# Optimization experiments

Hardware: AMD Instinct MI355X
Metric: run time of the kernel (lower is better)

The kernel has to match this reference:

```python
import jax, jax.numpy as jnp
import numpy as np

N = 100000
E = 1600000
IN_C, HID_C, OUT_C = 128, 128, 64
BN_EPS = 1e-5


def setup_inputs() -> dict:
    key = jax.random.key(0)
    ks = jax.random.split(key, 8)
    x = jax.random.normal(ks[0], (N, IN_C), dtype=jnp.float32)
    edge_index = jax.random.randint(ks[1], (2, E), 0, N, dtype=jnp.int64)
    # GCNConv: Linear(in, out, bias=False) + separate bias added after aggregation
    W1 = jax.random.normal(ks[2], (IN_C, HID_C), dtype=jnp.float32) / np.sqrt(IN_C)
    b1 = jnp.zeros((HID_C,), dtype=jnp.float32)
    gamma = jnp.ones((HID_C,), dtype=jnp.float32)
    beta = jnp.zeros((HID_C,), dtype=jnp.float32)
    W2 = jax.random.normal(ks[3], (HID_C, OUT_C), dtype=jnp.float32) / np.sqrt(HID_C)
    b2 = jnp.zeros((OUT_C,), dtype=jnp.float32)
    return {"x": x, "edge_index": edge_index, "W1": W1, "b1": b1,
            "gamma": gamma, "beta": beta, "W2": W2, "b2": b2}


def _gcn_norm(edge_index, n):
    # add self-loops, symmetric normalization deg^-1/2 * deg^-1/2 (PyG gcn_norm)
    loop = jnp.arange(n, dtype=edge_index.dtype)
    row = jnp.concatenate([edge_index[0], loop])  # source (j)
    col = jnp.concatenate([edge_index[1], loop])  # target (i)
    deg = jax.ops.segment_sum(jnp.ones_like(col, dtype=jnp.float32), col, num_segments=n)
    d_inv_sqrt = jnp.where(deg > 0, jax.lax.rsqrt(deg), 0.0)
    norm = d_inv_sqrt[row] * d_inv_sqrt[col]  # [E + N]
    return row, col, norm


def _gcn_conv(h, W, b, row, col, norm, n):
    h = h @ W                                        # [N, out]
    msg = h[row] * norm[:, None]                     # gather + scale  [E+N, out]
    agg = jax.ops.segment_sum(msg, col, num_segments=n)  # scatter-add [N, out]
    return agg + b


def _batchnorm(h, gamma, beta):
    mean = jnp.mean(h, axis=0)
    var = jnp.mean(jnp.square(h - mean), axis=0)
    return (h - mean) * jax.lax.rsqrt(var + BN_EPS) * gamma + beta


def reference(x, edge_index, W1, b1, gamma, beta, W2, b2):
    n = x.shape[0]
    row, col, norm = _gcn_norm(edge_index, n)
    h = _gcn_conv(x, W1, b1, row, col, norm, n)
    h = _batchnorm(h, gamma, beta)
    h = jax.nn.relu(h)
    # dropout is identity in deterministic/eval reference
    out = _gcn_conv(h, W2, b2, row, col, norm, n)
    return out
```

## Files before the change

kernel.cpp:

```cpp
#include <hip/hip_runtime.h>

#define IN_C 128
#define HID_C 128
#define OUT_C 64
#define BN_EPS 1e-5f
#define BUCK_SHIFT 6
#define MAXBUCK 2048

typedef unsigned short ushort_t;
typedef __attribute__((ext_vector_type(8))) short bf16x8;
typedef __attribute__((ext_vector_type(4))) float f32x4;
typedef __attribute__((ext_vector_type(8))) unsigned short u16x8;

__device__ __forceinline__ float bf2f(ushort_t u) {
  union { unsigned i; float f; } c; c.i = (unsigned)u << 16; return c.f;
}
__device__ __forceinline__ ushort_t f2bf(float f) {
  union { float f; unsigned u; } c; c.f = f;
  unsigned r = c.u + 0x7FFF + ((c.u >> 16) & 1);
  return (ushort_t)(r >> 16);
}


__global__ __launch_bounds__(256) void k_hist(const int* __restrict__ col,
                                              int* __restrict__ ghist,
                                              int e, int nbuck, int chunk) {
  __shared__ int h[MAXBUCK];
  for (int p = threadIdx.x; p < nbuck; p += 256) h[p] = 0;
  __syncthreads();
  int s = blockIdx.x * chunk;
  int t = min(s + chunk, e);
  for (int i = s + threadIdx.x; i < t; i += 256)
    atomicAdd(&h[col[i] >> BUCK_SHIFT], 1);
  __syncthreads();
  int* gh = ghist + (size_t)blockIdx.x * nbuck;
  for (int p = threadIdx.x; p < nbuck; p += 256) gh[p] = h[p];
}

__global__ __launch_bounds__(256) void k_s1(int* __restrict__ ghist,
                                            int* __restrict__ btotal, int nbuck) {
  __shared__ int sd[256];
  int p = blockIdx.x;
  int tid = threadIdx.x;
  int idx = tid * nbuck + p;
  int v = ghist[idx];
  sd[tid] = v;
  __syncthreads();
  for (int off = 1; off < 256; off <<= 1) {
    int t = (tid >= off) ? sd[tid - off] : 0;
    __syncthreads();
    sd[tid] += t;
    __syncthreads();
  }
  ghist[idx] = sd[tid] - v;
  if (tid == 255) btotal[p] = sd[255];
}

__global__ __launch_bounds__(512) void k_s2(const int* __restrict__ btotal,
                                            int* __restrict__ bstart,
                                            int nbuck, int e,
                                            int* __restrict__ rowptr, int n) {
  __shared__ int sd[512];
  int tid = threadIdx.x;
  int base = tid * 4;
  int v[4]; int s = 0;
#pragma unroll
  for (int q = 0; q < 4; q++) {
    int i = base + q;
    v[q] = (i < nbuck) ? btotal[i] : 0;
    s += v[q];
  }
  sd[tid] = s;
  __syncthreads();
  for (int off = 1; off < 512; off <<= 1) {
    int t = (tid >= off) ? sd[tid - off] : 0;
    __syncthreads();
    sd[tid] += t;
    __syncthreads();
  }
  int run = sd[tid] - s;
#pragma unroll
  for (int q = 0; q < 4; q++) {
    int i = base + q;
    if (i < nbuck) bstart[i] = run;
    run += v[q];
  }
  if (tid == 0) { bstart[nbuck] = e; rowptr[n] = e; }
}

__global__ __launch_bounds__(256) void k_scatter(const int* __restrict__ row,
                                                 const int* __restrict__ col,
                                                 const int* __restrict__ ghist,
                                                 const int* __restrict__ bstart,
                                                 unsigned* __restrict__ bpack,
                                                 int e, int nbuck, int chunk) {
  __shared__ int cur[MAXBUCK];
  const int* gh = ghist + (size_t)blockIdx.x * nbuck;
  for (int p = threadIdx.x; p < nbuck; p += 256) cur[p] = bstart[p] + gh[p];
  __syncthreads();
  int s = blockIdx.x * chunk;
  int t = min(s + chunk, e);
  for (int i = s + threadIdx.x; i < t; i += 256) {
    int c = col[i];
    int pos = atomicAdd(&cur[c >> BUCK_SHIFT], 1);
    bpack[pos] = ((unsigned)(c & 63) << 17) | (unsigned)row[i];
  }
}

__global__ __launch_bounds__(256) void k_bsort(const unsigned* __restrict__ bpack,
                                               const int* __restrict__ bstart,
                                               int* __restrict__ rowptr,
                                               float* __restrict__ dis,
                                               int* __restrict__ srcidx, int n) {
  __shared__ int cnt[64];
  __shared__ int pos[64];
  __shared__ int sbs, sbe;
  int tid = threadIdx.x;
  int p = blockIdx.x;
  if (tid < 64) cnt[tid] = 0;
  if (tid == 0) { sbs = bstart[p]; sbe = bstart[p + 1]; }
  __syncthreads();
  int bs = sbs, be = sbe;
  for (int i = bs + tid; i < be; i += 256)
    atomicAdd(&cnt[bpack[i] >> 17], 1);
  __syncthreads();
  if (tid < 64) {
    int v = cnt[tid];
    int run = v;
#pragma unroll
    for (int off = 1; off < 64; off <<= 1) {
      int o = __shfl_up(run, off, 64);
      if (tid >= off) run += o;
    }
    int excl = run - v;
    pos[tid] = excl;
    int node = (p << BUCK_SHIFT) + tid;
    if (node < n) {
      rowptr[node] = bs + excl;
      dis[node] = rsqrtf((float)(v + 1));
    }
  }
  __syncthreads();
  for (int i = bs + tid; i < be; i += 256) {
    unsigned v = bpack[i];
    int q = atomicAdd(&pos[v >> 17], 1);
    srcidx[bs + q] = (int)(v & 0x1FFFFu);
  }
}


__global__ void k_wpack(const float* __restrict__ W1, const float* __restrict__ W2,
                        ushort_t* __restrict__ WB1, ushort_t* __restrict__ WB2,
                        float* __restrict__ stats) {
  int idx = blockIdx.x * 256 + threadIdx.x;
  if (blockIdx.x == 0) stats[threadIdx.x] = 0.f;
  if (idx < 128 * 128) {
    int nn = idx >> 7, k = idx & 127;
    WB1[idx] = f2bf(W1[k * HID_C + nn]);
  }
  int idx2 = idx - 128 * 128;
  if (idx2 >= 0 && idx2 < 64 * 128) {
    int nn = idx2 >> 7, k = idx2 & 127;
    WB2[idx2] = f2bf(W2[k * OUT_C + nn]);
  }
}


__global__ __launch_bounds__(256) void k_gemm1_mfma(const float* __restrict__ x,
                                                    const ushort_t* __restrict__ WB,
                                                    ushort_t* __restrict__ h1, int n) {
  int wave = threadIdx.x >> 6;
  int lane = threadIdx.x & 63;
  int m = lane & 15;
  int kg = lane >> 4;
  int rowbase = blockIdx.x * 64 + wave * 16;
  int rrow = rowbase + m; if (rrow >= n) rrow = n - 1;
  const float* xrow = x + (size_t)rrow * IN_C + kg * 8;
  f32x4 acc[8] = {};
#pragma unroll
  for (int ks = 0; ks < 4; ks++) {
    float4 a0 = *reinterpret_cast<const float4*>(xrow + ks * 32);
    float4 a1 = *reinterpret_cast<const float4*>(xrow + ks * 32 + 4);
    bf16x8 a;
    a[0] = (short)f2bf(a0.x); a[1] = (short)f2bf(a0.y);
    a[2] = (short)f2bf(a0.z); a[3] = (short)f2bf(a0.w);
    a[4] = (short)f2bf(a1.x); a[5] = (short)f2bf(a1.y);
    a[6] = (short)f2bf(a1.z); a[7] = (short)f2bf(a1.w);
#pragma unroll
    for (int nt = 0; nt < 8; nt++) {
      bf16x8 b = *reinterpret_cast<const bf16x8*>(WB + (nt * 16 + m) * 128 + ks * 32 + kg * 8);
      acc[nt] = __builtin_amdgcn_mfma_f32_16x16x32_bf16(a, b, acc[nt], 0, 0, 0);
    }
  }
#pragma unroll
  for (int nt = 0; nt < 8; nt++)
#pragma unroll
    for (int r = 0; r < 4; r++) {
      int rowi = rowbase + kg * 4 + r;
      if (rowi < n) h1[(size_t)rowi * HID_C + nt * 16 + m] = f2bf(acc[nt][r]);
    }
}


__global__ __launch_bounds__(256) void k_gemm2_mfma(const ushort_t* __restrict__ aggb,
                                                    const ushort_t* __restrict__ WB,
                                                    const float* __restrict__ stats,
                                                    const float* __restrict__ gamma,
                                                    const float* __restrict__ beta,
                                                    ushort_t* __restrict__ h2, int n) {
  __shared__ float bnp_s[256];
  int tid = threadIdx.x;
  if (tid < 128) {
    float inv_n = 1.f / (float)n;
    float mean = stats[tid] * inv_n;
    float var = stats[128 + tid] * inv_n - mean * mean;
    float istd = rsqrtf(var + BN_EPS);
    float sc = gamma[tid] * istd;
    bnp_s[tid] = sc;
    bnp_s[128 + tid] = beta[tid] - mean * sc;
  }
  __syncthreads();
  int wave = tid >> 6;
  int lane = tid & 63;
  int m = lane & 15;
  int kg = lane >> 4;
  int rowbase = blockIdx.x * 64 + wave * 16;
  int rrow = rowbase + m; if (rrow >= n) rrow = n - 1;
  const ushort_t* arow = aggb + (size_t)rrow * HID_C + kg * 8;
  f32x4 acc[4] = {};
#pragma unroll
  for (int ks = 0; ks < 4; ks++) {
    int kbase = ks * 32 + kg * 8;
    u16x8 av = *reinterpret_cast<const u16x8*>(arow + ks * 32);
    float v[8];
#pragma unroll
    for (int q = 0; q < 8; q++)
      v[q] = bf2f(av[q]) * bnp_s[kbase + q] + bnp_s[128 + kbase + q];
    bf16x8 a;
#pragma unroll
    for (int q = 0; q < 8; q++) a[q] = (short)f2bf(v[q] > 0.f ? v[q] : 0.f);
#pragma unroll
    for (int nt = 0; nt < 4; nt++) {
      bf16x8 b = *reinterpret_cast<const bf16x8*>(WB + (nt * 16 + m) * 128 + ks * 32 + kg * 8);
      acc[nt] = __builtin_amdgcn_mfma_f32_16x16x32_bf16(a, b, acc[nt], 0, 0, 0);
    }
  }
#pragma unroll
  for (int nt = 0; nt < 4; nt++)
#pragma unroll
    for (int r = 0; r < 4; r++) {
      int rowi = rowbase + kg * 4 + r;
      if (rowi < n) h2[(size_t)rowi * OUT_C + nt * 16 + m] = f2bf(acc[nt][r]);
    }
}


__global__ __launch_bounds__(256) void k_spmm1_bf(const ushort_t* __restrict__ h,
                                                  const float* __restrict__ dis,
                                                  const int* __restrict__ rowptr,
                                                  const int* __restrict__ srcidx,
                                                  const float* __restrict__ bias,
                                                  ushort_t* __restrict__ outp, int n) {
  constexpr int C = HID_C;
  constexpr int LPR = C / 8;
  constexpr int ROWS = 256 / LPR;
  int tid = threadIdx.x;
  int lane = tid & (LPR - 1);
  int r = tid / LPR;
  int i = blockIdx.x * ROWS + r;
  if (i >= n) return;
  int c8 = lane * 8;
  const ushort_t* hb = h + c8;

  float di = dis[i];
  float acc[8];
  u16x8 hv = *reinterpret_cast<const u16x8*>(hb + (size_t)i * C);
#pragma unroll
  for (int q = 0; q < 8; q++) acc[q] = di * bf2f(hv[q]);

  int s = rowptr[i], t = rowptr[i + 1];
  int p = s;
  for (; p + 16 <= t; p += 16) {
    int jA[8], jB[8]; float dA[8], dB[8]; u16x8 vA[8], vB[8];
#pragma unroll
    for (int k = 0; k < 8; k++) jA[k] = srcidx[p + k];
#pragma unroll
    for (int k = 0; k < 8; k++) jB[k] = srcidx[p + 8 + k];
#pragma unroll
    for (int k = 0; k < 8; k++) dA[k] = dis[jA[k]];
#pragma unroll
    for (int k = 0; k < 8; k++) dB[k] = dis[jB[k]];
#pragma unroll
    for (int k = 0; k < 8; k++)
      vA[k] = *reinterpret_cast<const u16x8*>(hb + (size_t)jA[k] * C);
#pragma unroll
    for (int k = 0; k < 8; k++)
      vB[k] = *reinterpret_cast<const u16x8*>(hb + (size_t)jB[k] * C);
#pragma unroll
    for (int k = 0; k < 8; k++)
#pragma unroll
      for (int q = 0; q < 8; q++) acc[q] += dA[k] * bf2f(vA[k][q]);
#pragma unroll
    for (int k = 0; k < 8; k++)
#pragma unroll
      for (int q = 0; q < 8; q++) acc[q] += dB[k] * bf2f(vB[k][q]);
  }
  for (; p + 4 <= t; p += 4) {
    int j[4]; float dj[4]; u16x8 v[4];
#pragma unroll
    for (int k = 0; k < 4; k++) j[k] = srcidx[p + k];
#pragma unroll
    for (int k = 0; k < 4; k++) dj[k] = dis[j[k]];
#pragma unroll
    for (int k = 0; k < 4; k++)
      v[k] = *reinterpret_cast<const u16x8*>(hb + (size_t)j[k] * C);
#pragma unroll
    for (int k = 0; k < 4; k++)
#pragma unroll
      for (int q = 0; q < 8; q++) acc[q] += dj[k] * bf2f(v[k][q]);
  }
  for (; p < t; p++) {
    int j = srcidx[p];
    float dj = dis[j];
    u16x8 v = *reinterpret_cast<const u16x8*>(hb + (size_t)j * C);
#pragma unroll
    for (int q = 0; q < 8; q++) acc[q] += dj * bf2f(v[q]);
  }

  float4 b0 = *reinterpret_cast<const float4*>(bias + c8);
  float4 b1v = *reinterpret_cast<const float4*>(bias + c8 + 4);
  u16x8 o;
  o[0] = f2bf(di * acc[0] + b0.x);  o[1] = f2bf(di * acc[1] + b0.y);
  o[2] = f2bf(di * acc[2] + b0.z);  o[3] = f2bf(di * acc[3] + b0.w);
  o[4] = f2bf(di * acc[4] + b1v.x); o[5] = f2bf(di * acc[5] + b1v.y);
  o[6] = f2bf(di * acc[6] + b1v.z); o[7] = f2bf(di * acc[7] + b1v.w);
  *reinterpret_cast<u16x8*>(outp + (size_t)i * C + c8) = o;
}


__global__ __launch_bounds__(256) void k_spmm2_bf(const ushort_t* __restrict__ h,
                                                  const float* __restrict__ dis,
                                                  const int* __restrict__ rowptr,
                                                  const int* __restrict__ srcidx,
                                                  const float* __restrict__ bias,
                                                  float* __restrict__ outp, int n) {
  constexpr int C = OUT_C;
  constexpr int LPR = C / 8;
  constexpr int ROWS = 256 / LPR;
  int tid = threadIdx.x;
  int lane = tid & (LPR - 1);
  int r = tid / LPR;
  int i = blockIdx.x * ROWS + r;
  if (i >= n) return;
  int c8 = lane * 8;
  const ushort_t* hb = h + c8;

  float di = dis[i];
  float acc[8];
  u16x8 hv = *reinterpret_cast<const u16x8*>(hb + (size_t)i * C);
#pragma unroll
  for (int q = 0; q < 8; q++) acc[q] = di * bf2f(hv[q]);

  int s = rowptr[i], t = rowptr[i + 1];
  int p = s;
  for (; p + 16 <= t; p += 16) {
    int jA[8], jB[8]; float dA[8], dB[8]; u16x8 vA[8], vB[8];
#pragma unroll
    for (int k = 0; k < 8; k++) jA[k] = srcidx[p + k];
#pragma unroll
    for (int k = 0; k < 8; k++) jB[k] = srcidx[p + 8 + k];
#pragma unroll
    for (int k = 0; k < 8; k++) dA[k] = dis[jA[k]];
#pragma unroll
    for (int k = 0; k < 8; k++) dB[k] = dis[jB[k]];
#pragma unroll
    for (int k = 0; k < 8; k++)
      vA[k] = *reinterpret_cast<const u16x8*>(hb + (size_t)jA[k] * C);
#pragma unroll
    for (int k = 0; k < 8; k++)
      vB[k] = *reinterpret_cast<const u16x8*>(hb + (size_t)jB[k] * C);
#pragma unroll
    for (int k = 0; k < 8; k++)
#pragma unroll
      for (int q = 0; q < 8; q++) acc[q] += dA[k] * bf2f(vA[k][q]);
#pragma unroll
    for (int k = 0; k < 8; k++)
#pragma unroll
      for (int q = 0; q < 8; q++) acc[q] += dB[k] * bf2f(vB[k][q]);
  }
  for (; p + 4 <= t; p += 4) {
    int j[4]; float dj[4]; u16x8 v[4];
#pragma unroll
    for (int k = 0; k < 4; k++) j[k] = srcidx[p + k];
#pragma unroll
    for (int k = 0; k < 4; k++) dj[k] = dis[j[k]];
#pragma unroll
    for (int k = 0; k < 4; k++)
      v[k] = *reinterpret_cast<const u16x8*>(hb + (size_t)j[k] * C);
#pragma unroll
    for (int k = 0; k < 4; k++)
#pragma unroll
      for (int q = 0; q < 8; q++) acc[q] += dj[k] * bf2f(v[k][q]);
  }
  for (; p < t; p++) {
    int j = srcidx[p];
    float dj = dis[j];
    u16x8 v = *reinterpret_cast<const u16x8*>(hb + (size_t)j * C);
#pragma unroll
    for (int q = 0; q < 8; q++) acc[q] += dj * bf2f(v[q]);
  }

  float4 b0 = *reinterpret_cast<const float4*>(bias + c8);
  float4 b1v = *reinterpret_cast<const float4*>(bias + c8 + 4);
  float4 o0, o1;
  o0.x = di * acc[0] + b0.x;  o0.y = di * acc[1] + b0.y;
  o0.z = di * acc[2] + b0.z;  o0.w = di * acc[3] + b0.w;
  o1.x = di * acc[4] + b1v.x; o1.y = di * acc[5] + b1v.y;
  o1.z = di * acc[6] + b1v.z; o1.w = di * acc[7] + b1v.w;
  float* op = outp + (size_t)i * C + c8;
  *reinterpret_cast<float4*>(op) = o0;
  *reinterpret_cast<float4*>(op + 4) = o1;
}


__global__ __launch_bounds__(256) void k_bnstats(const ushort_t* __restrict__ aggb,
                                                 float* __restrict__ stats, int n) {
  __shared__ float lsum[256 * 8];
  __shared__ float lsq[256 * 8];
  int tid = threadIdx.x;
  int lane = tid & 15;
  int rg = tid >> 4;
  float s[8] = {}, q[8] = {};
  for (int row = blockIdx.x * 16 + rg; row < n; row += gridDim.x * 16) {
    u16x8 v = *reinterpret_cast<const u16x8*>(aggb + (size_t)row * HID_C + lane * 8);
#pragma unroll
    for (int k = 0; k < 8; k++) {
      float f = bf2f(v[k]);
      s[k] += f;
      q[k] += f * f;
    }
  }
#pragma unroll
  for (int k = 0; k < 8; k++) { lsum[tid * 8 + k] = s[k]; lsq[tid * 8 + k] = q[k]; }
  __syncthreads();
  if (tid < 128) {
    int ln = tid >> 3, k = tid & 7;
    float ss = 0.f, qq = 0.f;
    for (int r = 0; r < 16; r++) {
      int idx = ((r << 4) + ln) * 8 + k;
      ss += lsum[idx];
      qq += lsq[idx];
    }
    atomicAdd(&stats[tid], ss);
    atomicAdd(&stats[128 + tid], qq);
  }
}


extern "C" void kernel_launch(void* const* d_in, const int* in_sizes, int n_in,
                              void* d_out, int out_size, void* d_ws, size_t ws_size,
                              hipStream_t stream) {
  const float* x     = (const float*)d_in[0];
  const int*   edge  = (const int*)d_in[1];
  const float* W1    = (const float*)d_in[2];
  const float* b1    = (const float*)d_in[3];
  const float* gamma = (const float*)d_in[4];
  const float* beta  = (const float*)d_in[5];
  const float* W2    = (const float*)d_in[6];
  const float* b2    = (const float*)d_in[7];
  float* out = (float*)d_out;

  int n = in_sizes[0] / IN_C;
  int e = in_sizes[1] / 2;
  int n64 = ((n + 63) / 64) * 64;
  int nbuck = (n + 63) >> BUCK_SHIFT;
  const int* row = edge;
  const int* col = edge + e;

  char* ws = (char*)d_ws;
  size_t off = 0;
  auto alloc = [&](size_t bytes) {
    void* p = ws + off;
    off = (off + bytes + 255) & ~(size_t)255;
    return p;
  };
  float*    dis   = (float*)alloc((size_t)n * 4);
  int*      rowp  = (int*)alloc((size_t)(n + 1) * 4);
  int*      srci  = (int*)alloc((size_t)e * 4);
  ushort_t* WB1   = (ushort_t*)alloc(128 * 128 * 2);
  ushort_t* WB2   = (ushort_t*)alloc(64 * 128 * 2);
  ushort_t* h1b   = (ushort_t*)alloc((size_t)n64 * HID_C * 2);
  ushort_t* aggb  = (ushort_t*)alloc((size_t)n64 * HID_C * 2);
  ushort_t* h2b   = (ushort_t*)alloc((size_t)n64 * OUT_C * 2);
  float*    stats = (float*)alloc(256 * 4);
  char* tr = (char*)aggb;
  unsigned* bpack = (unsigned*)tr;                       tr += (size_t)e * 4;
  int* ghist  = (int*)tr;                                tr += (size_t)256 * nbuck * 4;
  int* btotal = (int*)tr;                                tr += (size_t)(nbuck + 1) * 4;
  int* bstart = (int*)tr;
  (void)ws_size; (void)n_in; (void)out_size;

  int chunk = (e + 255) / 256;
  int nb64 = n64 / 64;

  k_wpack  <<<96, 256, 0, stream>>>(W1, W2, WB1, WB2, stats);
  k_hist   <<<256, 256, 0, stream>>>(col, ghist, e, nbuck, chunk);
  k_s1     <<<nbuck, 256, 0, stream>>>(ghist, btotal, nbuck);
  k_s2     <<<1, 512, 0, stream>>>(btotal, bstart, nbuck, e, rowp, n);
  k_scatter<<<256, 256, 0, stream>>>(row, col, ghist, bstart, bpack, e, nbuck, chunk);
  k_bsort  <<<nbuck, 256, 0, stream>>>(bpack, bstart, rowp, dis, srci, n);
  k_gemm1_mfma<<<nb64, 256, 0, stream>>>(x, WB1, h1b, n);
  k_spmm1_bf<<<(n + 15) / 16, 256, 0, stream>>>(h1b, dis, rowp, srci, b1, aggb, n);
  k_bnstats<<<512, 256, 0, stream>>>(aggb, stats, n);
  k_gemm2_mfma<<<nb64, 256, 0, stream>>>(aggb, WB2, stats, gamma, beta, h2b, n);
  k_spmm2_bf<<<(n + 31) / 32, 256, 0, stream>>>(h2b, dis, rowp, srci, b2, out, n);
}
```

Baseline: 240.2 us.

## Store features in 16-column slices and prescale rows by source degree norm

Hidden and output features now use a column-sliced layout: separate contiguous arrays of 16 bf16 columns per node. Each SpMM block handles one slice, so the gathered working set per pass is 16x smaller and more likely to stay in cache. The GEMM epilogues multiply each row by its source d^-1/2, which removes the per-edge dis[j] gather from the SpMM loops. The cost is that each edge index list is re-read once per slice, and every kernel indexes with the new slice strides.

```diff
diff --git a/kernel.cpp b/kernel.cpp
--- a/kernel.cpp
+++ b/kernel.cpp
@@ -168,7 +168,9 @@
 
 __global__ __launch_bounds__(256) void k_gemm1_mfma(const float* __restrict__ x,
                                                     const ushort_t* __restrict__ WB,
-                                                    ushort_t* __restrict__ h1, int n) {
+                                                    const float* __restrict__ dis,
+                                                    ushort_t* __restrict__ h1c,
+                                                    int n, int n64) {
   int wave = threadIdx.x >> 6;
   int lane = threadIdx.x & 63;
   int m = lane & 15;
@@ -192,13 +194,17 @@
       acc[nt] = __builtin_amdgcn_mfma_f32_16x16x32_bf16(a, b, acc[nt], 0, 0, 0);
     }
   }
-#pragma unroll
-  for (int nt = 0; nt < 8; nt++)
-#pragma unroll
-    for (int r = 0; r < 4; r++) {
-      int rowi = rowbase + kg * 4 + r;
-      if (rowi < n) h1[(size_t)rowi * HID_C + nt * 16 + m] = f2bf(acc[nt][r]);
-    }
+  size_t slice = (size_t)n64 * 16;
+#pragma unroll
+  for (int r = 0; r < 4; r++) {
+    int rowi = rowbase + kg * 4 + r;
+    if (rowi < n) {
+      float dr = dis[rowi];
+#pragma unroll
+      for (int nt = 0; nt < 8; nt++)
+        h1c[(size_t)nt * slice + (size_t)rowi * 16 + m] = f2bf(dr * acc[nt][r]);
+    }
+  }
 }
 
 
@@ -207,7 +213,9 @@
                                                     const float* __restrict__ stats,
                                                     const float* __restrict__ gamma,
                                                     const float* __restrict__ beta,
-                                                    ushort_t* __restrict__ h2, int n) {
+                                                    const float* __restrict__ dis,
+                                                    ushort_t* __restrict__ h2c,
+                                                    int n, int n64) {
   __shared__ float bnp_s[256];
   int tid = threadIdx.x;
   if (tid < 128) {
@@ -226,12 +234,14 @@
   int kg = lane >> 4;
   int rowbase = blockIdx.x * 64 + wave * 16;
   int rrow = rowbase + m; if (rrow >= n) rrow = n - 1;
-  const ushort_t* arow = aggb + (size_t)rrow * HID_C + kg * 8;
+  size_t slice = (size_t)n64 * 16;
   f32x4 acc[4] = {};
 #pragma unroll
   for (int ks = 0; ks < 4; ks++) {
     int kbase = ks * 32 + kg * 8;
-    u16x8 av = *reinterpret_cast<const u16x8*>(arow + ks * 32);
+    int gA = ks * 2 + (kg >> 1);
+    u16x8 av = *reinterpret_cast<const u16x8*>(aggb + (size_t)gA * slice +
+                                               (size_t)rrow * 16 + (kg & 1) * 8);
     float v[8];
 #pragma unroll
     for (int q = 0; q < 8; q++)
@@ -246,193 +256,168 @@
     }
   }
 #pragma unroll
-  for (int nt = 0; nt < 4; nt++)
-#pragma unroll
-    for (int r = 0; r < 4; r++) {
-      int rowi = rowbase + kg * 4 + r;
-      if (rowi < n) h2[(size_t)rowi * OUT_C + nt * 16 + m] = f2bf(acc[nt][r]);
-    }
-}
-
-
-__global__ __launch_bounds__(256) void k_spmm1_bf(const ushort_t* __restrict__ h,
-                                                  const float* __restrict__ dis,
+  for (int r = 0; r < 4; r++) {
+    int rowi = rowbase + kg * 4 + r;
+    if (rowi < n) {
+      float dr = dis[rowi];
+#pragma unroll
+      for (int nt = 0; nt < 4; nt++)
+        h2c[(size_t)nt * slice + (size_t)rowi * 16 + m] = f2bf(dr * acc[nt][r]);
+    }
+  }
+}
+
+
+__global__ __launch_bounds__(256) void k_spmm1_bf(const ushort_t* __restrict__ h1c,
                                                   const int* __restrict__ rowptr,
                                                   const int* __restrict__ srcidx,
                                                   const float* __restrict__ bias,
-                                                  ushort_t* __restrict__ outp, int n) {
-  constexpr int C = HID_C;
-  constexpr int LPR = C / 8;
-  constexpr int ROWS = 256 / LPR;
-  int tid = threadIdx.x;
-  int lane = tid & (LPR - 1);
-  int r = tid / LPR;
-  int i = blockIdx.x * ROWS + r;
+                                                  const float* __restrict__ dis,
+                                                  ushort_t* __restrict__ aggb,
+                                                  int n, int n64) {
+  int tid = threadIdx.x;
+  int g = blockIdx.x & 7;
+  int i = (blockIdx.x >> 3) * 128 + (tid >> 1);
   if (i >= n) return;
-  int c8 = lane * 8;
-  const ushort_t* hb = h + c8;
-
-  float di = dis[i];
+  int lane8 = (tid & 1) * 8;
+  size_t slice = (size_t)n64 * 16;
+  const ushort_t* hb = h1c + (size_t)g * slice + lane8;
+
   float acc[8];
-  u16x8 hv = *reinterpret_cast<const u16x8*>(hb + (size_t)i * C);
-#pragma unroll
-  for (int q = 0; q < 8; q++) acc[q] = di * bf2f(hv[q]);
+  u16x8 hv = *reinterpret_cast<const u16x8*>(hb + (size_t)i * 16);
+#pragma unroll
+  for (int q = 0; q < 8; q++) acc[q] = bf2f(hv[q]);
 
   int s = rowptr[i], t = rowptr[i + 1];
   int p = s;
   for (; p + 16 <= t; p += 16) {
-    int jA[8], jB[8]; float dA[8], dB[8]; u16x8 vA[8], vB[8];
-#pragma unroll
-    for (int k = 0; k < 8; k++) jA[k] = srcidx[p + k];
-#pragma unroll
-    for (int k = 0; k < 8; k++) jB[k] = srcidx[p + 8 + k];
-#pragma unroll
-    for (int k = 0; k < 8; k++) dA[k] = dis[jA[k]];
-#pragma unroll
-    for (int k = 0; k < 8; k++) dB[k] = dis[jB[k]];
-#pragma unroll
-    for (int k = 0; k < 8; k++)
-      vA[k] = *reinterpret_cast<const u16x8*>(hb + (size_t)jA[k] * C);
-#pragma unroll
-    for (int k = 0; k < 8; k++)
-      vB[k] = *reinterpret_cast<const u16x8*>(hb + (size_t)jB[k] * C);
-#pragma unroll
-    for (int k = 0; k < 8; k++)
-#pragma unroll
-      for (int q = 0; q < 8; q++) acc[q] += dA[k] * bf2f(vA[k][q]);
-#pragma unroll
-    for (int k = 0; k < 8; k++)
-#pragma unroll
-      for (int q = 0; q < 8; q++) acc[q] += dB[k] * bf2f(vB[k][q]);
+    int j[16]; u16x8 v[16];
+#pragma unroll
+    for (int k = 0; k < 16; k++) j[k] = srcidx[p + k];
+#pragma unroll
+    for (int k = 0; k < 16; k++)
+      v[k] = *reinterpret_cast<const u16x8*>(hb + (size_t)j[k] * 16);
+#pragma unroll
+    for (int k = 0; k < 16; k++)
+#pragma unroll
+      for (int q = 0; q < 8; q++) acc[q] += bf2f(v[k][q]);
   }
   for (; p + 4 <= t; p += 4) {
-    int j[4]; float dj[4]; u16x8 v[4];
+    int j[4]; u16x8 v[4];
 #pragma unroll
     for (int k = 0; k < 4; k++) j[k] = srcidx[p + k];
 #pragma unroll
-    for (int k = 0; k < 4; k++) dj[k] = dis[j[k]];
-#pragma unroll
     for (int k = 0; k < 4; k++)
-      v[k] = *reinterpret_cast<const u16x8*>(hb + (size_t)j[k] * C);
+      v[k] = *reinterpret_cast<const u16x8*>(hb + (size_t)j[k] * 16);
 #pragma unroll
     for (int k = 0; k < 4; k++)
 #pragma unroll
-      for (int q = 0; q < 8; q++) acc[q] += dj[k] * bf2f(v[k][q]);
+      for (int q = 0; q < 8; q++) acc[q] += bf2f(v[k][q]);
   }
   for (; p < t; p++) {
     int j = srcidx[p];
-    float dj = dis[j];
-    u16x8 v = *reinterpret_cast<const u16x8*>(hb + (size_t)j * C);
-#pragma unroll
-    for (int q = 0; q < 8; q++) acc[q] += dj * bf2f(v[q]);
-  }
-
-  float4 b0 = *reinterpret_cast<const float4*>(bias + c8);
-  float4 b1v = *reinterpret_cast<const float4*>(bias + c8 + 4);
+    u16x8 v = *reinterpret_cast<const u16x8*>(hb + (size_t)j * 16);
+#pragma unroll
+    for (int q = 0; q < 8; q++) acc[q] += bf2f(v[q]);
+  }
+
+  float di = dis[i];
+  int cb = g * 16 + lane8;
+  float4 b0 = *reinterpret_cast<const float4*>(bias + cb);
+  float4 b1v = *reinterpret_cast<const float4*>(bias + cb + 4);
   u16x8 o;
   o[0] = f2bf(di * acc[0] + b0.x);  o[1] = f2bf(di * acc[1] + b0.y);
   o[2] = f2bf(di * acc[2] + b0.z);  o[3] = f2bf(di * acc[3] + b0.w);
   o[4] = f2bf(di * acc[4] + b1v.x); o[5] = f2bf(di * acc[5] + b1v.y);
   o[6] = f2bf(di * acc[6] + b1v.z); o[7] = f2bf(di * acc[7] + b1v.w);
-  *reinterpret_cast<u16x8*>(outp + (size_t)i * C + c8) = o;
-}
-
-
-__global__ __launch_bounds__(256) void k_spmm2_bf(const ushort_t* __restrict__ h,
-                                                  const float* __restrict__ dis,
+  *reinterpret_cast<u16x8*>(aggb + (size_t)g * slice + (size_t)i * 16 + lane8) = o;
+}
+
+
+__global__ __launch_bounds__(256) void k_spmm2_bf(const ushort_t* __restrict__ h2c,
                                                   const int* __restrict__ rowptr,
                                                   const int* __restrict__ srcidx,
                                                   const float* __restrict__ bias,
-                                                  float* __restrict__ outp, int n) {
-  constexpr int C = OUT_C;
-  constexpr int LPR = C / 8;
-  constexpr int ROWS = 256 / LPR;
-  int tid = threadIdx.x;
-  int lane = tid & (LPR - 1);
-  int r = tid / LPR;
-  int i = blockIdx.x * ROWS + r;
+                                                  const float* __restrict__ dis,
+                                                  float* __restrict__ outp,
+                                                  int n, int n64) {
+  int tid = threadIdx.x;
+  int s8 = blockIdx.x & 7;
+  int g = s8 & 3;
+  int chunk = (blockIdx.x >> 3) * 2 + (s8 >> 2);
+  int i = chunk * 128 + (tid >> 1);
   if (i >= n) return;
-  int c8 = lane * 8;
-  const ushort_t* hb = h + c8;
-
-  float di = dis[i];
+  int lane8 = (tid & 1) * 8;
+  size_t slice = (size_t)n64 * 16;
+  const ushort_t* hb = h2c + (size_t)g * slice + lane8;
+
   float acc[8];
-  u16x8 hv = *reinterpret_cast<const u16x8*>(hb + (size_t)i * C);
-#pragma unroll
-  for (int q = 0; q < 8; q++) acc[q] = di * bf2f(hv[q]);
+  u16x8 hv = *reinterpret_cast<const u16x8*>(hb + (size_t)i * 16);
+#pragma unroll
+  for (int q = 0; q < 8; q++) acc[q] = bf2f(hv[q]);
 
   int s = rowptr[i], t = rowptr[i + 1];
   int p = s;
   for (; p + 16 <= t; p += 16) {
-    int jA[8], jB[8]; float dA[8], dB[8]; u16x8 vA[8], vB[8];
-#pragma unroll
-    for (int k = 0; k < 8; k++) jA[k] = srcidx[p + k];
-#pragma unroll
-    for (int k = 0; k < 8; k++) jB[k] = srcidx[p + 8 + k];
-#pragma unroll
-    for (int k = 0; k < 8; k++) dA[k] = dis[jA[k]];
-#pragma unroll
-    for (int k = 0; k < 8; k++) dB[k] = dis[jB[k]];
-#pragma unroll
-    for (int k = 0; k < 8; k++)
-      vA[k] = *reinterpret_cast<const u16x8*>(hb + (size_t)jA[k] * C);
-#pragma unroll
-    for (int k = 0; k < 8; k++)
-      vB[k] = *reinterpret_cast<const u16x8*>(hb + (size_t)jB[k] * C);
-#pragma unroll
-    for (int k = 0; k < 8; k++)
-#pragma unroll
-      for (int q = 0; q < 8; q++) acc[q] += dA[k] * bf2f(vA[k][q]);
-#pragma unroll
-    for (int k = 0; k < 8; k++)
-#pragma unroll
-      for (int q = 0; q < 8; q++) acc[q] += dB[k] * bf2f(vB[k][q]);
+    int j[16]; u16x8 v[16];
+#pragma unroll
+    for (int k = 0; k < 16; k++) j[k] = srcidx[p + k];
+#pragma unroll
+    for (int k = 0; k < 16; k++)
+      v[k] = *reinterpret_cast<const u16x8*>(hb + (size_t)j[k] * 16);
+#pragma unroll
+    for (int k = 0; k < 16; k++)
+#pragma unroll
+      for (int q = 0; q < 8; q++) acc[q] += bf2f(v[k][q]);
   }
   for (; p + 4 <= t; p += 4) {
-    int j[4]; float dj[4]; u16x8 v[4];
+    int j[4]; u16x8 v[4];
 #pragma unroll
     for (int k = 0; k < 4; k++) j[k] = srcidx[p + k];
 #pragma unroll
-    for (int k = 0; k < 4; k++) dj[k] = dis[j[k]];
-#pragma unroll
     for (int k = 0; k < 4; k++)
-      v[k] = *reinterpret_cast<const u16x8*>(hb + (size_t)j[k] * C);
+      v[k] = *reinterpret_cast<const u16x8*>(hb + (size_t)j[k] * 16);
 #pragma unroll
     for (int k = 0; k < 4; k++)
 #pragma unroll
-      for (int q = 0; q < 8; q++) acc[q] += dj[k] * bf2f(v[k][q]);
+      for (int q = 0; q < 8; q++) acc[q] += bf2f(v[k][q]);
   }
   for (; p < t; p++) {
     int j = srcidx[p];
-    float dj = dis[j];
-    u16x8 v = *reinterpret_cast<const u16x8*>(hb + (size_t)j * C);
-#pragma unroll
-    for (int q = 0; q < 8; q++) acc[q] += dj * bf2f(v[q]);
-  }
-
-  float4 b0 = *reinterpret_cast<const float4*>(bias + c8);
-  float4 b1v = *reinterpret_cast<const float4*>(bias + c8 + 4);
+    u16x8 v = *reinterpret_cast<const u16x8*>(hb + (size_t)j * 16);
+#pragma unroll
+    for (int q = 0; q < 8; q++) acc[q] += bf2f(v[q]);
+  }
+
+  float di = dis[i];
+  int cb = g * 16 + lane8;
+  float4 b0 = *reinterpret_cast<const float4*>(bias + cb);
+  float4 b1v = *reinterpret_cast<const float4*>(bias + cb + 4);
   float4 o0, o1;
   o0.x = di * acc[0] + b0.x;  o0.y = di * acc[1] + b0.y;
   o0.z = di * acc[2] + b0.z;  o0.w = di * acc[3] + b0.w;
   o1.x = di * acc[4] + b1v.x; o1.y = di * acc[5] + b1v.y;
   o1.z = di * acc[6] + b1v.z; o1.w = di * acc[7] + b1v.w;
-  float* op = outp + (size_t)i * C + c8;
+  float* op = outp + (size_t)i * OUT_C + cb;
   *reinterpret_cast<float4*>(op) = o0;
   *reinterpret_cast<float4*>(op + 4) = o1;
 }
 
 
 __global__ __launch_bounds__(256) void k_bnstats(const ushort_t* __restrict__ aggb,
-                                                 float* __restrict__ stats, int n) {
-  __shared__ float lsum[256 * 8];
-  __shared__ float lsq[256 * 8];
-  int tid = threadIdx.x;
-  int lane = tid & 15;
-  int rg = tid >> 4;
+                                                 float* __restrict__ stats,
+                                                 int n, int n64) {
+  __shared__ float ls[8][256];
+  __shared__ float lq2[8][256];
+  int tid = threadIdx.x;
+  int g = blockIdx.x & 7;
+  int lane8 = (tid & 1) * 8;
+  size_t slice = (size_t)n64 * 16;
+  const ushort_t* base = aggb + (size_t)g * slice + lane8;
+  int stride = (gridDim.x >> 3) * 128;
   float s[8] = {}, q[8] = {};
-  for (int row = blockIdx.x * 16 + rg; row < n; row += gridDim.x * 16) {
-    u16x8 v = *reinterpret_cast<const u16x8*>(aggb + (size_t)row * HID_C + lane * 8);
+  for (int i = (blockIdx.x >> 3) * 128 + (tid >> 1); i < n; i += stride) {
+    u16x8 v = *reinterpret_cast<const u16x8*>(base + (size_t)i * 16);
 #pragma unroll
     for (int k = 0; k < 8; k++) {
       float f = bf2f(v[k]);
@@ -441,18 +426,25 @@
     }
   }
 #pragma unroll
-  for (int k = 0; k < 8; k++) { lsum[tid * 8 + k] = s[k]; lsq[tid * 8 + k] = q[k]; }
-  __syncthreads();
-  if (tid < 128) {
-    int ln = tid >> 3, k = tid & 7;
-    float ss = 0.f, qq = 0.f;
-    for (int r = 0; r < 16; r++) {
-      int idx = ((r << 4) + ln) * 8 + k;
-      ss += lsum[idx];
-      qq += lsq[idx];
-    }
-    atomicAdd(&stats[tid], ss);
-    atomicAdd(&stats[128 + tid], qq);
+  for (int k = 0; k < 8; k++) { ls[k][tid] = s[k]; lq2[k][tid] = q[k]; }
+  for (int off = 128; off >= 2; off >>= 1) {
+    __syncthreads();
+    if (tid < off) {
+#pragma unroll
+      for (int k = 0; k < 8; k++) {
+        ls[k][tid] += ls[k][tid + off];
+        lq2[k][tid] += lq2[k][tid + off];
+      }
+    }
+  }
+  __syncthreads();
+  if (tid < 2) {
+    int cb = g * 16 + tid * 8;
+#pragma unroll
+    for (int k = 0; k < 8; k++) {
+      atomicAdd(&stats[cb + k], ls[k][tid]);
+      atomicAdd(&stats[128 + cb + k], lq2[k][tid]);
+    }
   }
 }
 
@@ -489,9 +481,9 @@
   int*      srci  = (int*)alloc((size_t)e * 4);
   ushort_t* WB1   = (ushort_t*)alloc(128 * 128 * 2);
   ushort_t* WB2   = (ushort_t*)alloc(64 * 128 * 2);
-  ushort_t* h1b   = (ushort_t*)alloc((size_t)n64 * HID_C * 2);
+  ushort_t* h1c   = (ushort_t*)alloc((size_t)n64 * HID_C * 2);
   ushort_t* aggb  = (ushort_t*)alloc((size_t)n64 * HID_C * 2);
-  ushort_t* h2b   = (ushort_t*)alloc((size_t)n64 * OUT_C * 2);
+  ushort_t* h2c   = (ushort_t*)alloc((size_t)n64 * OUT_C * 2);
   float*    stats = (float*)alloc(256 * 4);
   char* tr = (char*)aggb;
   unsigned* bpack = (unsigned*)tr;                       tr += (size_t)e * 4;
@@ -502,6 +494,9 @@
 
   int chunk = (e + 255) / 256;
   int nb64 = n64 / 64;
+  int nb128 = (n + 127) / 128;
+  int grid_spmm1 = 8 * nb128;
+  int grid_spmm2 = 8 * ((nb128 + 1) / 2);
 
   k_wpack  <<<96, 256, 0, stream>>>(W1, W2, WB1, WB2, stats);
   k_hist   <<<256, 256, 0, stream>>>(col, ghist, e, nbuck, chunk);
@@ -509,9 +504,9 @@
   k_s2     <<<1, 512, 0, stream>>>(btotal, bstart, nbuck, e, rowp, n);
   k_scatter<<<256, 256, 0, stream>>>(row, col, ghist, bstart, bpack, e, nbuck, chunk);
   k_bsort  <<<nbuck, 256, 0, stream>>>(bpack, bstart, rowp, dis, srci, n);
-  k_gemm1_mfma<<<nb64, 256, 0, stream>>>(x, WB1, h1b, n);
-  k_spmm1_bf<<<(n + 15) / 16, 256, 0, stream>>>(h1b, dis, rowp, srci, b1, aggb, n);
-  k_bnstats<<<512, 256, 0, stream>>>(aggb, stats, n);
-  k_gemm2_mfma<<<nb64, 256, 0, stream>>>(aggb, WB2, stats, gamma, beta, h2b, n);
-  k_spmm2_bf<<<(n + 31) / 32, 256, 0, stream>>>(h2b, dis, rowp, srci, b2, out, n);
-}
+  k_gemm1_mfma<<<nb64, 256, 0, stream>>>(x, WB1, dis, h1c, n, n64);
+  k_spmm1_bf<<<grid_spmm1, 256, 0, stream>>>(h1c, rowp, srci, b1, dis, aggb, n, n64);
+  k_bnstats<<<512, 256, 0, stream>>>(aggb, stats, n, n64);
+  k_gemm2_mfma<<<nb64, 256, 0, stream>>>(aggb, WB2, stats, gamma, beta, dis, h2c, n, n64);
+  k_spmm2_bf<<<grid_spmm2, 256, 0, stream>>>(h2c, rowp, srci, b2, dis, out, n, n64);
+}
```

New measurement: 263.4 us. 9.7% more time.

## Fold source-degree scaling into GEMM epilogues and sort CSR neighbors by source chunk

Applied to the files above, without the earlier changes.

The d^-1/2 factor of each source node is now applied once per row in the GEMM epilogues, so the SpMM inner loops no longer gather dis[j] for every edge and do plain sums instead of scaled FMAs. The bucket sort now keys on (target, source>>13), so each node's neighbor list is grouped by source region, aiming for better cache locality in the gathers. The trade is a larger shared-memory histogram and a multi-barrier block-wide scan in k_bsort, and the scaled values are rounded to bf16 before aggregation.

```diff
diff --git a/kernel.cpp b/kernel.cpp
--- a/kernel.cpp
+++ b/kernel.cpp
@@ -6,6 +6,7 @@
 #define BN_EPS 1e-5f
 #define BUCK_SHIFT 6
 #define MAXBUCK 2048
+#define CHUNK_SHIFT 13
 
 typedef unsigned short ushort_t;
 typedef __attribute__((ext_vector_type(8))) short bf16x8;
@@ -112,38 +113,54 @@
                                                int* __restrict__ rowptr,
                                                float* __restrict__ dis,
                                                int* __restrict__ srcidx, int n) {
-  __shared__ int cnt[64];
-  __shared__ int pos[64];
+  __shared__ int cnt[1024];
+  __shared__ int excl[1025];
+  __shared__ int sd[256];
   __shared__ int sbs, sbe;
   int tid = threadIdx.x;
   int p = blockIdx.x;
-  if (tid < 64) cnt[tid] = 0;
+  for (int q = tid; q < 1024; q += 256) cnt[q] = 0;
   if (tid == 0) { sbs = bstart[p]; sbe = bstart[p + 1]; }
   __syncthreads();
   int bs = sbs, be = sbe;
-  for (int i = bs + tid; i < be; i += 256)
-    atomicAdd(&cnt[bpack[i] >> 17], 1);
+  for (int i = bs + tid; i < be; i += 256) {
+    unsigned v = bpack[i];
+    int key = (int)((v >> 17) << 4) | (int)((v & 0x1FFFFu) >> CHUNK_SHIFT);
+    atomicAdd(&cnt[key], 1);
+  }
+  __syncthreads();
+  int base = tid * 4;
+  int c0 = cnt[base], c1 = cnt[base + 1], c2 = cnt[base + 2], c3 = cnt[base + 3];
+  int s = c0 + c1 + c2 + c3;
+  sd[tid] = s;
+  __syncthreads();
+  for (int off = 1; off < 256; off <<= 1) {
+    int t = (tid >= off) ? sd[tid - off] : 0;
+    __syncthreads();
+    sd[tid] += t;
+    __syncthreads();
+  }
+  int run = sd[tid] - s;
+  excl[base] = run;
+  excl[base + 1] = run + c0;
+  excl[base + 2] = run + c0 + c1;
+  excl[base + 3] = run + c0 + c1 + c2;
+  if (tid == 255) excl[1024] = sd[255];
   __syncthreads();
   if (tid < 64) {
-    int v = cnt[tid];
-    int run = v;
-#pragma unroll
-    for (int off = 1; off < 64; off <<= 1) {
-      int o = __shfl_up(run, off, 64);
-      if (tid >= off) run += o;
-    }
-    int excl = run - v;
-    pos[tid] = excl;
+    int st = excl[tid * 16];
+    int en = excl[(tid + 1) * 16];
     int node = (p << BUCK_SHIFT) + tid;
     if (node < n) {
-      rowptr[node] = bs + excl;
-      dis[node] = rsqrtf((float)(v + 1));
+      rowptr[node] = bs + st;
+      dis[node] = rsqrtf((float)(en - st + 1));
     }
   }
   __syncthreads();
   for (int i = bs + tid; i < be; i += 256) {
     unsigned v = bpack[i];
-    int q = atomicAdd(&pos[v >> 17], 1);
+    int key = (int)((v >> 17) << 4) | (int)((v & 0x1FFFFu) >> CHUNK_SHIFT);
+    int q = atomicAdd(&excl[key], 1);
     srcidx[bs + q] = (int)(v & 0x1FFFFu);
   }
 }
@@ -168,6 +185,7 @@
 
 __global__ __launch_bounds__(256) void k_gemm1_mfma(const float* __restrict__ x,
                                                     const ushort_t* __restrict__ WB,
+                                                    const float* __restrict__ dis,
                                                     ushort_t* __restrict__ h1, int n) {
   int wave = threadIdx.x >> 6;
   int lane = threadIdx.x & 63;
@@ -193,12 +211,15 @@
     }
   }
 #pragma unroll
-  for (int nt = 0; nt < 8; nt++)
-#pragma unroll
-    for (int r = 0; r < 4; r++) {
-      int rowi = rowbase + kg * 4 + r;
-      if (rowi < n) h1[(size_t)rowi * HID_C + nt * 16 + m] = f2bf(acc[nt][r]);
-    }
+  for (int r = 0; r < 4; r++) {
+    int rowi = rowbase + kg * 4 + r;
+    if (rowi < n) {
+      float dr = dis[rowi];
+#pragma unroll
+      for (int nt = 0; nt < 8; nt++)
+        h1[(size_t)rowi * HID_C + nt * 16 + m] = f2bf(dr * acc[nt][r]);
+    }
+  }
 }
 
 
@@ -207,6 +228,7 @@
                                                     const float* __restrict__ stats,
                                                     const float* __restrict__ gamma,
                                                     const float* __restrict__ beta,
+                                                    const float* __restrict__ dis,
                                                     ushort_t* __restrict__ h2, int n) {
   __shared__ float bnp_s[256];
   int tid = threadIdx.x;
@@ -246,12 +268,15 @@
     }
   }
 #pragma unroll
-  for (int nt = 0; nt < 4; nt++)
-#pragma unroll
-    for (int r = 0; r < 4; r++) {
-      int rowi = rowbase + kg * 4 + r;
-      if (rowi < n) h2[(size_t)rowi * OUT_C + nt * 16 + m] = f2bf(acc[nt][r]);
-    }
+  for (int r = 0; r < 4; r++) {
+    int rowi = rowbase + kg * 4 + r;
+    if (rowi < n) {
+      float dr = dis[rowi];
+#pragma unroll
+      for (int nt = 0; nt < 4; nt++)
+        h2[(size_t)rowi * OUT_C + nt * 16 + m] = f2bf(dr * acc[nt][r]);
+    }
+  }
 }
 
 
@@ -272,61 +297,45 @@
   int c8 = lane * 8;
   const ushort_t* hb = h + c8;
 
-  float di = dis[i];
   float acc[8];
   u16x8 hv = *reinterpret_cast<const u16x8*>(hb + (size_t)i * C);
 #pragma unroll
-  for (int q = 0; q < 8; q++) acc[q] = di * bf2f(hv[q]);
+  for (int q = 0; q < 8; q++) acc[q] = bf2f(hv[q]);
 
   int s = rowptr[i], t = rowptr[i + 1];
   int p = s;
   for (; p + 16 <= t; p += 16) {
-    int jA[8], jB[8]; float dA[8], dB[8]; u16x8 vA[8], vB[8];
-#pragma unroll
-    for (int k = 0; k < 8; k++) jA[k] = srcidx[p + k];
-#pragma unroll
-    for (int k = 0; k < 8; k++) jB[k] = srcidx[p + 8 + k];
-#pragma unroll
-    for (int k = 0; k < 8; k++) dA[k] = dis[jA[k]];
-#pragma unroll
-    for (int k = 0; k < 8; k++) dB[k] = dis[jB[k]];
-#pragma unroll
-    for (int k = 0; k < 8; k++)
-      vA[k] = *reinterpret_cast<const u16x8*>(hb + (size_t)jA[k] * C);
-#pragma unroll
-    for (int k = 0; k < 8; k++)
-      vB[k] = *reinterpret_cast<const u16x8*>(hb + (size_t)jB[k] * C);
-#pragma unroll
-    for (int k = 0; k < 8; k++)
-#pragma unroll
-      for (int q = 0; q < 8; q++) acc[q] += dA[k] * bf2f(vA[k][q]);
-#pragma unroll
-    for (int k = 0; k < 8; k++)
-#pragma unroll
-      for (int q = 0; q < 8; q++) acc[q] += dB[k] * bf2f(vB[k][q]);
+    int j[16]; u16x8 v[16];
+#pragma unroll
+    for (int k = 0; k < 16; k++) j[k] = srcidx[p + k];
+#pragma unroll
+    for (int k = 0; k < 16; k++)
+      v[k] = *reinterpret_cast<const u16x8*>(hb + (size_t)j[k] * C);
+#pragma unroll
+    for (int k = 0; k < 16; k++)
+#pragma unroll
+      for (int q = 0; q < 8; q++) acc[q] += bf2f(v[k][q]);
   }
   for (; p + 4 <= t; p += 4) {
-    int j[4]; float dj[4]; u16x8 v[4];
+    int j[4]; u16x8 v[4];
 #pragma unroll
     for (int k = 0; k < 4; k++) j[k] = srcidx[p + k];
-#pragma unroll
-    for (int k = 0; k < 4; k++) dj[k] = dis[j[k]];
 #pragma unroll
     for (int k = 0; k < 4; k++)
       v[k] = *reinterpret_cast<const u16x8*>(hb + (size_t)j[k] * C);
 #pragma unroll
     for (int k = 0; k < 4; k++)
 #pragma unroll
-      for (int q = 0; q < 8; q++) acc[q] += dj[k] * bf2f(v[k][q]);
+      for (int q = 0; q < 8; q++) acc[q] += bf2f(v[k][q]);
   }
   for (; p < t; p++) {
     int j = srcidx[p];
-    float dj = dis[j];
     u16x8 v = *reinterpret_cast<const u16x8*>(hb + (size_t)j * C);
 #pragma unroll
-    for (int q = 0; q < 8; q++) acc[q] += dj * bf2f(v[q]);
-  }
-
+    for (int q = 0; q < 8; q++) acc[q] += bf2f(v[q]);
+  }
+
+  float di = dis[i];
   float4 b0 = *reinterpret_cast<const float4*>(bias + c8);
   float4 b1v = *reinterpret_cast<const float4*>(bias + c8 + 4);
   u16x8 o;
@@ -355,61 +364,45 @@
   int c8 = lane * 8;
   const ushort_t* hb = h + c8;
 
-  float di = dis[i];
   float acc[8];
   u16x8 hv = *reinterpret_cast<const u16x8*>(hb + (size_t)i * C);
 #pragma unroll
-  for (int q = 0; q < 8; q++) acc[q] = di * bf2f(hv[q]);
+  for (int q = 0; q < 8; q++) acc[q] = bf2f(hv[q]);
 
   int s = rowptr[i], t = rowptr[i + 1];
   int p = s;
   for (; p + 16 <= t; p += 16) {
-    int jA[8], jB[8]; float dA[8], dB[8]; u16x8 vA[8], vB[8];
-#pragma unroll
-    for (int k = 0; k < 8; k++) jA[k] = srcidx[p + k];
-#pragma unroll
-    for (int k = 0; k < 8; k++) jB[k] = srcidx[p + 8 + k];
-#pragma unroll
-    for (int k = 0; k < 8; k++) dA[k] = dis[jA[k]];
-#pragma unroll
-    for (int k = 0; k < 8; k++) dB[k] = dis[jB[k]];
-#pragma unroll
-    for (int k = 0; k < 8; k++)
-      vA[k] = *reinterpret_cast<const u16x8*>(hb + (size_t)jA[k] * C);
-#pragma unroll
-    for (int k = 0; k < 8; k++)
-      vB[k] = *reinterpret_cast<const u16x8*>(hb + (size_t)jB[k] * C);
-#pragma unroll
-    for (int k = 0; k < 8; k++)
-#pragma unroll
-      for (int q = 0; q < 8; q++) acc[q] += dA[k] * bf2f(vA[k][q]);
-#pragma unroll
-    for (int k = 0; k < 8; k++)
-#pragma unroll
-      for (int q = 0; q < 8; q++) acc[q] += dB[k] * bf2f(vB[k][q]);
+    int j[16]; u16x8 v[16];
+#pragma unroll
+    for (int k = 0; k < 16; k++) j[k] = srcidx[p + k];
+#pragma unroll
+    for (int k = 0; k < 16; k++)
+      v[k] = *reinterpret_cast<const u16x8*>(hb + (size_t)j[k] * C);
+#pragma unroll
+    for (int k = 0; k < 16; k++)
+#pragma unroll
+      for (int q = 0; q < 8; q++) acc[q] += bf2f(v[k][q]);
   }
   for (; p + 4 <= t; p += 4) {
-    int j[4]; float dj[4]; u16x8 v[4];
+    int j[4]; u16x8 v[4];
 #pragma unroll
     for (int k = 0; k < 4; k++) j[k] = srcidx[p + k];
-#pragma unroll
-    for (int k = 0; k < 4; k++) dj[k] = dis[j[k]];
 #pragma unroll
     for (int k = 0; k < 4; k++)
       v[k] = *reinterpret_cast<const u16x8*>(hb + (size_t)j[k] * C);
 #pragma unroll
     for (int k = 0; k < 4; k++)
 #pragma unroll
-      for (int q = 0; q < 8; q++) acc[q] += dj[k] * bf2f(v[k][q]);
+      for (int q = 0; q < 8; q++) acc[q] += bf2f(v[k][q]);
   }
   for (; p < t; p++) {
     int j = srcidx[p];
-    float dj = dis[j];
     u16x8 v = *reinterpret_cast<const u16x8*>(hb + (size_t)j * C);
 #pragma unroll
-    for (int q = 0; q < 8; q++) acc[q] += dj * bf2f(v[q]);
-  }
-
+    for (int q = 0; q < 8; q++) acc[q] += bf2f(v[q]);
+  }
+
+  float di = dis[i];
   float4 b0 = *reinterpret_cast<const float4*>(bias + c8);
   float4 b1v = *reinterpret_cast<const float4*>(bias + c8 + 4);
   float4 o0, o1;
@@ -509,9 +502,9 @@
   k_s2     <<<1, 512, 0, stream>>>(btotal, bstart, nbuck, e, rowp, n);
   k_scatter<<<256, 256, 0, stream>>>(row, col, ghist, bstart, bpack, e, nbuck, chunk);
   k_bsort  <<<nbuck, 256, 0, stream>>>(bpack, bstart, rowp, dis, srci, n);
-  k_gemm1_mfma<<<nb64, 256, 0, stream>>>(x, WB1, h1b, n);
+  k_gemm1_mfma<<<nb64, 256, 0, stream>>>(x, WB1, dis, h1b, n);
   k_spmm1_bf<<<(n + 15) / 16, 256, 0, stream>>>(h1b, dis, rowp, srci, b1, aggb, n);
   k_bnstats<<<512, 256, 0, stream>>>(aggb, stats, n);
-  k_gemm2_mfma<<<nb64, 256, 0, stream>>>(aggb, WB2, stats, gamma, beta, h2b, n);
+  k_gemm2_mfma<<<nb64, 256, 0, stream>>>(aggb, WB2, stats, gamma, beta, dis, h2b, n);
   k_spmm2_bf<<<(n + 31) / 32, 256, 0, stream>>>(h2b, dis, rowp, srci, b2, out, n);
 }
```

New measurement: 231.0 us. -3.8%, faster.
